# Kernel tuning notes

Hardware: AMD Instinct MI355X
Metric: run time of the kernel (lower is better)

## Reference

```python
import jax, jax.numpy as jnp
from jax import lax
import numpy as np

NUM_CAPS = 4
CAP_DIM = 8
NUM_CLASSES = 10
CLASS_DIM = 16


def squash(x):
    # x: [..., D]; scale = |x|^2/(1+|x|^2)/sqrt(|x|^2+1e-8)
    sq = jnp.sum(x * x, axis=-1, keepdims=True)
    return sq / (1.0 + sq) / jnp.sqrt(sq + 1e-8) * x


def primary_caps(x, w, b):
    # x: [B,C,H,W], w: [32,C,3,3] -> caps [B, H*W*NUM_CAPS, CAP_DIM]
    out = lax.conv_general_dilated(
        x, w, window_strides=(1, 1), padding=[(1, 1), (1, 1)],
        dimension_numbers=('NCHW', 'OIHW', 'NCHW')) + b[None, :, None, None]
    B, C, H, W = out.shape
    out = out.reshape(B, NUM_CAPS, CAP_DIM, H * W)
    out = out.transpose(0, 3, 1, 2).reshape(B, H * W * NUM_CAPS, CAP_DIM)
    return squash(out)


def setup_inputs() -> dict:
    key = jax.random.key(0)
    ks = jax.random.split(key, 7)
    B, H, Wd = 64, 32, 32
    hsi_c, sar_c = 144, 4
    N = 2 * H * Wd * NUM_CAPS  # 8192
    return {
        'x_hsi': jax.random.normal(ks[0], (B, hsi_c, H, Wd), jnp.float32),
        'x_sar': jax.random.normal(ks[1], (B, sar_c, H, Wd), jnp.float32),
        'wh': jax.random.normal(ks[2], (NUM_CAPS * CAP_DIM, hsi_c, 3, 3), jnp.float32) * 0.05,
        'bh': jax.random.normal(ks[3], (NUM_CAPS * CAP_DIM,), jnp.float32) * 0.05,
        'ws': jax.random.normal(ks[4], (NUM_CAPS * CAP_DIM, sar_c, 3, 3), jnp.float32) * 0.05,
        'bs': jax.random.normal(ks[5], (NUM_CAPS * CAP_DIM,), jnp.float32) * 0.05,
        'W': jax.random.normal(ks[6], (N, NUM_CLASSES, CLASS_DIM, CAP_DIM), jnp.float32),
    }


def reference(x_hsi, x_sar, wh, bh, ws, bs, W):
    caps_h = primary_caps(x_hsi, wh, bh)
    caps_s = primary_caps(x_sar, ws, bs)
    caps = jnp.concatenate([caps_h, caps_s], axis=1)  # [B, N, D]
    N = caps.shape[1]
    # routing_iters=1 with b=0 => c = 1/N uniform; s = sum_n c*u_hat = mean_n u_hat
    # u_hat[b,n,c,j] = sum_d W[n,c,j,d] * caps[b,n,d] (fused, never materialized)
    s = jnp.einsum('bnd,ncjd->bcj', caps, W) / N  # [B, num_classes, class_dim]
    v = squash(s)
    logits = jnp.sqrt(jnp.sum(v * v, axis=-1))  # [B, num_classes]
    return logits
```

## Files before the change

kernel.cpp:

```cpp
#include <hip/hip_runtime.h>
#include <hip/hip_bf16.h>


typedef __attribute__((ext_vector_type(8))) short bf16x8s;
typedef __attribute__((ext_vector_type(4))) float f32x4;

__device__ inline short f2bf(float f) {
    __hip_bfloat16 h = __float2bfloat16(f);
    return *reinterpret_cast<short*>(&h);
}

#define XPLANE 1156
#define XB_B (20 * XPLANE * 8)

__global__ __launch_bounds__(256) void prep_kernel(
        const float* __restrict__ wh, short* __restrict__ wtb2,
        const float* __restrict__ x_hsi, short* __restrict__ xb2,
        const float* __restrict__ wsar, float* __restrict__ wt_s) {
    int t = threadIdx.x;
    if (blockIdx.x < 180) {
        int idx = blockIdx.x * 256 + t;
        int tap = idx / 5120;
        int r2 = idx - tap * 5120;
        int cb = r2 >> 8;
        int oc = (r2 >> 3) & 31;
        int d = r2 & 7;
        int ch = cb * 8 + d;
        short v = 0;
        if (ch < 144) v = f2bf(wh[(oc * 144 + ch) * 9 + tap]);
        wtb2[idx] = v;
        return;
    }
    if (blockIdx.x == 2356) {
        for (int idx = t; idx < 1152; idx += 256) {
            int oc = idx & 31;
            int rest = idx >> 5;
            int tap = rest % 9;
            int cin = rest / 9;
            wt_s[cin * 288 + tap * 32 + oc] = wsar[(oc * 4 + cin) * 9 + tap];
        }
        return;
    }
    int blk = blockIdx.x - 180;
    int b = blk / 34;
    int y_o = blk - b * 34;
    bool yok = (y_o >= 1) && (y_o <= 32);
    int iy = y_o - 1;
    short* dstb = xb2 + (size_t)b * XB_B;
    for (int item = t; item < 680; item += 256) {
        int cb = item / 34;
        int xx = item - cb * 34;
        bf16x8s v = {0, 0, 0, 0, 0, 0, 0, 0};
        if (yok && xx >= 1 && xx <= 32 && cb < 18) {
            int x = xx - 1;
            #pragma unroll
            for (int d = 0; d < 8; ++d) {
                int ch = cb * 8 + d;
                v[d] = f2bf(x_hsi[(((size_t)b * 144 + ch) * 32 + iy) * 32 + x]);
            }
        }
        *(bf16x8s*)(dstb + ((size_t)(cb * 34 + y_o) * 34 + xx) * 8) = v;
    }
}

__global__ __launch_bounds__(256) void conv_both_kernel(
        const float* __restrict__ x_sar, const short* __restrict__ xb2,
        const short* __restrict__ wtb2, const float* __restrict__ bh,
        const float* __restrict__ wt_s, const float* __restrict__ bs,
        short* __restrict__ capsb) {
    __shared__ float ct[64][34];
    int t = threadIdx.x;

    if (blockIdx.x < 1024) {
        int l = t & 63;
        int wv = t >> 6;
        int mhalf = wv >> 1;
        int nt = wv & 1;
        int l15 = l & 15, lhi = l >> 4;
        int b = blockIdx.x >> 4;
        int y0 = (blockIdx.x & 15) << 1;
        int y = y0 + mhalf;

        const short* xaBase = xb2 + (size_t)b * XB_B + (size_t)lhi * XPLANE * 8;
        const short* waBase = wtb2 + (size_t)lhi * 256 + (size_t)(nt * 16 + l15) * 8;

        f32x4 acc0 = {0.f, 0.f, 0.f, 0.f};
        f32x4 acc1 = {0.f, 0.f, 0.f, 0.f};

        #pragma unroll
        for (int tap = 0; tap < 9; ++tap) {
            int dy = tap / 3, dx = tap % 3;
            int pixoff = ((y + dy) * 34 + l15 + dx) * 8;
            #pragma unroll
            for (int kc = 0; kc < 5; ++kc) {
                const short* xa = xaBase + (size_t)kc * (4 * XPLANE * 8) + pixoff;
                bf16x8s a0 = *(const bf16x8s*)xa;
                bf16x8s a1 = *(const bf16x8s*)(xa + 16 * 8);
                bf16x8s bf = *(const bf16x8s*)(waBase + (size_t)(tap * 20 + kc * 4) * 256);
                acc0 = __builtin_amdgcn_mfma_f32_16x16x32_bf16(a0, bf, acc0, 0, 0, 0);
                acc1 = __builtin_amdgcn_mfma_f32_16x16x32_bf16(a1, bf, acc1, 0, 0, 0);
            }
        }

        #pragma unroll
        for (int r = 0; r < 4; ++r) {
            ct[mhalf * 32 + lhi * 4 + r][nt * 16 + l15] = acc0[r];
            ct[mhalf * 32 + 16 + lhi * 4 + r][nt * 16 + l15] = acc1[r];
        }
        __syncthreads();

        int p = t >> 2;
        int cap = t & 3;
        float s[8];
        float sq = 0.0f;
        #pragma unroll
        for (int d = 0; d < 8; ++d) {
            s[d] = ct[p][cap * 8 + d] + bh[cap * 8 + d];
            sq += s[d] * s[d];
        }
        float scale = sq / ((1.0f + sq) * sqrtf(sq + 1e-8f));
        int pix = (y0 + (p >> 5)) * 32 + (p & 31);
        int n = pix * 4 + cap;
        bf16x8s o;
        #pragma unroll
        for (int d = 0; d < 8; ++d) o[d] = f2bf(s[d] * scale);
        *(bf16x8s*)(capsb + ((size_t)b * 8192 + n) * 8) = o;
    } else {
        int px_global = (blockIdx.x - 1024) * 256 + t;
        int b = px_global >> 10;
        int p = px_global & 1023;
        int y = p >> 5, x = p & 31;

        float acc[32];
        #pragma unroll
        for (int oc = 0; oc < 32; ++oc) acc[oc] = bs[oc];

        for (int cin = 0; cin < 4; ++cin) {
            const float* xc = x_sar + ((size_t)b * 4 + cin) * 1024;
            const float* wc = wt_s + cin * 288;
            #pragma unroll
            for (int ky = 0; ky < 3; ++ky) {
                int iy = y + ky - 1;
                bool rowok = (iy >= 0) && (iy < 32);
                const float* xrow = xc + iy * 32;
                float v0 = (rowok && x > 0)  ? xrow[x - 1] : 0.0f;
                float v1 = rowok             ? xrow[x]     : 0.0f;
                float v2 = (rowok && x < 31) ? xrow[x + 1] : 0.0f;
                const float* wk = wc + ky * 96;
                #pragma unroll
                for (int oc = 0; oc < 32; ++oc)
                    acc[oc] += v0 * wk[oc] + v1 * wk[32 + oc] + v2 * wk[64 + oc];
            }
        }

        #pragma unroll
        for (int cap = 0; cap < 4; ++cap) {
            float sq = 0.0f;
            #pragma unroll
            for (int d = 0; d < 8; ++d) sq += acc[cap * 8 + d] * acc[cap * 8 + d];
            float scale = sq / ((1.0f + sq) * sqrtf(sq + 1e-8f));
            int n = 4096 + p * 4 + cap;
            bf16x8s o;
            #pragma unroll
            for (int d = 0; d < 8; ++d) o[d] = f2bf(acc[cap * 8 + d] * scale);
            *(bf16x8s*)(capsb + ((size_t)b * 8192 + n) * 8) = o;
        }
    }
}

__global__ __launch_bounds__(256) void routing_mfma_kernel(
        const short* __restrict__ capsb, const float* __restrict__ W,
        float* __restrict__ partials) {
    __shared__ union {
        short ct[32][64][8];
        float red[4][64][32];
    } sm;
    int t = threadIdx.x;
    int kc = blockIdx.x;
    int ntp = blockIdx.y;
    int n0 = kc * 32;

    {
        int b = t >> 2;
        int ng = t & 3;
        const short* src = capsb + ((size_t)b * 8192 + n0 + ng * 8) * 8;
        #pragma unroll
        for (int i = 0; i < 8; ++i) {
            bf16x8s v = *(const bf16x8s*)(src + i * 8);
            *(bf16x8s*)&sm.ct[ng * 8 + i][b][0] = v;
        }
    }
    __syncthreads();

    int l = t & 63;
    int wv = t >> 6;
    int l15 = l & 15, lhi = l >> 4;

    f32x4 acc[2][4];
    #pragma unroll
    for (int a = 0; a < 2; ++a)
        #pragma unroll
        for (int m = 0; m < 4; ++m) acc[a][m] = (f32x4){0.f, 0.f, 0.f, 0.f};

    #pragma unroll
    for (int ks = 0; ks < 2; ++ks) {
        int nl = (wv * 2 + ks) * 4 + lhi;
        int n = n0 + nl;
        const float* wp = W + ((size_t)n * 160 + ntp * 32 + l15) * 8;
        union { short s[8]; bf16x8s v; } bu[2];
        #pragma unroll
        for (int ntl = 0; ntl < 2; ++ntl) {
            const float* wq = wp + (size_t)ntl * 128;
            float4 w0 = *(const float4*)wq;
            float4 w1 = *(const float4*)(wq + 4);
            bu[ntl].s[0] = f2bf(w0.x); bu[ntl].s[1] = f2bf(w0.y);
            bu[ntl].s[2] = f2bf(w0.z); bu[ntl].s[3] = f2bf(w0.w);
            bu[ntl].s[4] = f2bf(w1.x); bu[ntl].s[5] = f2bf(w1.y);
            bu[ntl].s[6] = f2bf(w1.z); bu[ntl].s[7] = f2bf(w1.w);
        }
        bf16x8s af[4];
        #pragma unroll
        for (int mt = 0; mt < 4; ++mt)
            af[mt] = *(const bf16x8s*)&sm.ct[nl][mt * 16 + l15][0];
        #pragma unroll
        for (int ntl = 0; ntl < 2; ++ntl)
            #pragma unroll
            for (int mt = 0; mt < 4; ++mt)
                acc[ntl][mt] = __builtin_amdgcn_mfma_f32_16x16x32_bf16(
                    af[mt], bu[ntl].v, acc[ntl][mt], 0, 0, 0);
    }
    __syncthreads();

    #pragma unroll
    for (int ntl = 0; ntl < 2; ++ntl)
        #pragma unroll
        for (int mt = 0; mt < 4; ++mt)
            #pragma unroll
            for (int r = 0; r < 4; ++r)
                sm.red[wv][mt * 16 + lhi * 4 + r][ntl * 16 + l15] = acc[ntl][mt][r];
    __syncthreads();

    for (int idx = t; idx < 2048; idx += 256) {
        int b = idx >> 5, cjl = idx & 31;
        float sum = sm.red[0][b][cjl] + sm.red[1][b][cjl]
                  + sm.red[2][b][cjl] + sm.red[3][b][cjl];
        partials[(((size_t)kc * 5 + ntp) * 64 + b) * 32 + cjl] = sum;
    }
}

__global__ __launch_bounds__(256) void finalize_kernel(
        const float* __restrict__ partials, float* __restrict__ out) {
    __shared__ float s_sh[160];
    int t = threadIdx.x;
    int b = blockIdx.x;
    if (t < 160) {
        int ntp = t >> 5, cjl = t & 31;
        float s = 0.0f;
        #pragma unroll 8
        for (int kc = 0; kc < 256; ++kc)
            s += partials[(((size_t)kc * 5 + ntp) * 64 + b) * 32 + cjl];
        s_sh[ntp * 32 + cjl] = s * (1.0f / 8192.0f);
    }
    __syncthreads();
    if (t < 10) {
        float sq = 0.0f;
        #pragma unroll
        for (int j = 0; j < 16; ++j) {
            float v = s_sh[t * 16 + j];
            sq += v * v;
        }
        float scale = sq / ((1.0f + sq) * sqrtf(sq + 1e-8f));
        out[b * 10 + t] = sqrtf(sq) * scale;
    }
}

extern "C" void kernel_launch(void* const* d_in, const int* in_sizes, int n_in,
                              void* d_out, int out_size, void* d_ws, size_t ws_size,
                              hipStream_t stream) {
    const float* x_hsi = (const float*)d_in[0];
    const float* x_sar = (const float*)d_in[1];
    const float* wh    = (const float*)d_in[2];
    const float* bh    = (const float*)d_in[3];
    const float* wsar  = (const float*)d_in[4];
    const float* bs    = (const float*)d_in[5];
    const float* W     = (const float*)d_in[6];
    float* out = (float*)d_out;

    char* ws = (char*)d_ws;
    short* wtb2     = (short*)(ws + 0);
    float* wt_s     = (float*)(ws + 98304);
    short* xb2      = (short*)(ws + 131072);
    float* partials = (float*)(ws + 131072);
    short* capsb    = (short*)(ws + 23805952);

    prep_kernel<<<2357, 256, 0, stream>>>(wh, wtb2, x_hsi, xb2, wsar, wt_s);

    conv_both_kernel<<<1280, 256, 0, stream>>>(x_sar, xb2, wtb2, bh, wt_s, bs, capsb);

    routing_mfma_kernel<<<dim3(256, 5), 256, 0, stream>>>(capsb, W, partials);

    finalize_kernel<<<64, 256, 0, stream>>>(partials, out);
}
```

Before: 77.78 us.

## Stage conv input halo in LDS and retile HSI conv to 4 rows per block

```diff
diff --git a/kernel.cpp b/kernel.cpp
--- a/kernel.cpp
+++ b/kernel.cpp
@@ -17,6 +17,7 @@
         const float* __restrict__ wh, short* __restrict__ wtb2,
         const float* __restrict__ x_hsi, short* __restrict__ xb2,
         const float* __restrict__ wsar, float* __restrict__ wt_s) {
+    __shared__ short tile[144][33];
     int t = threadIdx.x;
     if (blockIdx.x < 180) {
         int idx = blockIdx.x * 256 + t;
@@ -46,6 +47,13 @@
     int y_o = blk - b * 34;
     bool yok = (y_o >= 1) && (y_o <= 32);
     int iy = y_o - 1;
+    if (yok) {
+        for (int base = 0; base < 144; base += 8) {
+            int ch = base + (t >> 5), x = t & 31;
+            tile[ch][x] = f2bf(x_hsi[(((size_t)b * 144 + ch) * 32 + iy) * 32 + x]);
+        }
+    }
+    __syncthreads();
     short* dstb = xb2 + (size_t)b * XB_B;
     for (int item = t; item < 680; item += 256) {
         int cb = item / 34;
@@ -54,10 +62,7 @@
         if (yok && xx >= 1 && xx <= 32 && cb < 18) {
             int x = xx - 1;
             #pragma unroll
-            for (int d = 0; d < 8; ++d) {
-                int ch = cb * 8 + d;
-                v[d] = f2bf(x_hsi[(((size_t)b * 144 + ch) * 32 + iy) * 32 + x]);
-            }
+            for (int d = 0; d < 8; ++d) v[d] = tile[cb * 8 + d][x];
         }
         *(bf16x8s*)(dstb + ((size_t)(cb * 34 + y_o) * 34 + xx) * 8) = v;
     }
@@ -68,65 +73,83 @@
         const short* __restrict__ wtb2, const float* __restrict__ bh,
         const float* __restrict__ wt_s, const float* __restrict__ bs,
         short* __restrict__ capsb) {
-    __shared__ float ct[64][34];
+    __shared__ union {
+        short xs[20][6][34][8];
+        float ct[128][33];
+    } sm;
     int t = threadIdx.x;
 
-    if (blockIdx.x < 1024) {
+    if (blockIdx.x < 512) {
+        int b = blockIdx.x >> 3;
+        int y0 = (blockIdx.x & 7) << 2;
+
+        const short* src = xb2 + (size_t)b * XB_B;
+        for (int i = t; i < 4080; i += 256) {
+            int cb = i / 204;
+            int rem = i - cb * 204;
+            int row = rem / 34;
+            int xx = rem - row * 34;
+            bf16x8s v = *(const bf16x8s*)(src + ((size_t)(cb * 34 + y0 + row) * 34 + xx) * 8);
+            *(bf16x8s*)&sm.xs[cb][row][xx][0] = v;
+        }
+        __syncthreads();
+
         int l = t & 63;
         int wv = t >> 6;
-        int mhalf = wv >> 1;
-        int nt = wv & 1;
         int l15 = l & 15, lhi = l >> 4;
-        int b = blockIdx.x >> 4;
-        int y0 = (blockIdx.x & 15) << 1;
-        int y = y0 + mhalf;
-
-        const short* xaBase = xb2 + (size_t)b * XB_B + (size_t)lhi * XPLANE * 8;
-        const short* waBase = wtb2 + (size_t)lhi * 256 + (size_t)(nt * 16 + l15) * 8;
-
-        f32x4 acc0 = {0.f, 0.f, 0.f, 0.f};
-        f32x4 acc1 = {0.f, 0.f, 0.f, 0.f};
+
+        f32x4 acc[2][2] = {{{0.f,0.f,0.f,0.f},{0.f,0.f,0.f,0.f}},
+                           {{0.f,0.f,0.f,0.f},{0.f,0.f,0.f,0.f}}};
 
         #pragma unroll
         for (int tap = 0; tap < 9; ++tap) {
             int dy = tap / 3, dx = tap % 3;
-            int pixoff = ((y + dy) * 34 + l15 + dx) * 8;
             #pragma unroll
             for (int kc = 0; kc < 5; ++kc) {
-                const short* xa = xaBase + (size_t)kc * (4 * XPLANE * 8) + pixoff;
-                bf16x8s a0 = *(const bf16x8s*)xa;
-                bf16x8s a1 = *(const bf16x8s*)(xa + 16 * 8);
-                bf16x8s bf = *(const bf16x8s*)(waBase + (size_t)(tap * 20 + kc * 4) * 256);
-                acc0 = __builtin_amdgcn_mfma_f32_16x16x32_bf16(a0, bf, acc0, 0, 0, 0);
-                acc1 = __builtin_amdgcn_mfma_f32_16x16x32_bf16(a1, bf, acc1, 0, 0, 0);
+                bf16x8s a0 = *(const bf16x8s*)&sm.xs[kc * 4 + lhi][wv + dy][l15 + dx][0];
+                bf16x8s a1 = *(const bf16x8s*)&sm.xs[kc * 4 + lhi][wv + dy][16 + l15 + dx][0];
+                const short* wa = wtb2 + ((size_t)(tap * 20 + kc * 4 + lhi) * 32 + l15) * 8;
+                bf16x8s b0 = *(const bf16x8s*)wa;
+                bf16x8s b1 = *(const bf16x8s*)(wa + 128);
+                acc[0][0] = __builtin_amdgcn_mfma_f32_16x16x32_bf16(a0, b0, acc[0][0], 0, 0, 0);
+                acc[0][1] = __builtin_amdgcn_mfma_f32_16x16x32_bf16(a0, b1, acc[0][1], 0, 0, 0);
+                acc[1][0] = __builtin_amdgcn_mfma_f32_16x16x32_bf16(a1, b0, acc[1][0], 0, 0, 0);
+                acc[1][1] = __builtin_amdgcn_mfma_f32_16x16x32_bf16(a1, b1, acc[1][1], 0, 0, 0);
             }
         }
-
-        #pragma unroll
-        for (int r = 0; r < 4; ++r) {
-            ct[mhalf * 32 + lhi * 4 + r][nt * 16 + l15] = acc0[r];
-            ct[mhalf * 32 + 16 + lhi * 4 + r][nt * 16 + l15] = acc1[r];
-        }
         __syncthreads();
 
-        int p = t >> 2;
-        int cap = t & 3;
-        float s[8];
-        float sq = 0.0f;
-        #pragma unroll
-        for (int d = 0; d < 8; ++d) {
-            s[d] = ct[p][cap * 8 + d] + bh[cap * 8 + d];
-            sq += s[d] * s[d];
-        }
-        float scale = sq / ((1.0f + sq) * sqrtf(sq + 1e-8f));
-        int pix = (y0 + (p >> 5)) * 32 + (p & 31);
-        int n = pix * 4 + cap;
-        bf16x8s o;
-        #pragma unroll
-        for (int d = 0; d < 8; ++d) o[d] = f2bf(s[d] * scale);
-        *(bf16x8s*)(capsb + ((size_t)b * 8192 + n) * 8) = o;
+        #pragma unroll
+        for (int xh = 0; xh < 2; ++xh)
+            #pragma unroll
+            for (int nt = 0; nt < 2; ++nt)
+                #pragma unroll
+                for (int r = 0; r < 4; ++r)
+                    sm.ct[wv * 32 + xh * 16 + lhi * 4 + r][nt * 16 + l15] = acc[xh][nt][r];
+        __syncthreads();
+
+        #pragma unroll
+        for (int h = 0; h < 2; ++h) {
+            int q = t + h * 256;
+            int p = q >> 2;
+            int cap = q & 3;
+            float s[8];
+            float sq = 0.0f;
+            #pragma unroll
+            for (int d = 0; d < 8; ++d) {
+                s[d] = sm.ct[p][cap * 8 + d] + bh[cap * 8 + d];
+                sq += s[d] * s[d];
+            }
+            float scale = sq / ((1.0f + sq) * sqrtf(sq + 1e-8f));
+            int pix = (y0 + (p >> 5)) * 32 + (p & 31);
+            int n = pix * 4 + cap;
+            bf16x8s o;
+            #pragma unroll
+            for (int d = 0; d < 8; ++d) o[d] = f2bf(s[d] * scale);
+            *(bf16x8s*)(capsb + ((size_t)b * 8192 + n) * 8) = o;
+        }
     } else {
-        int px_global = (blockIdx.x - 1024) * 256 + t;
+        int px_global = (blockIdx.x - 512) * 256 + t;
         int b = px_global >> 10;
         int p = px_global & 1023;
         int y = p >> 5, x = p & 31;
@@ -295,7 +318,7 @@
 
     prep_kernel<<<2357, 256, 0, stream>>>(wh, wtb2, x_hsi, xb2, wsar, wt_s);
 
-    conv_both_kernel<<<1280, 256, 0, stream>>>(x_sar, xb2, wtb2, bh, wt_s, bs, capsb);
+    conv_both_kernel<<<768, 256, 0, stream>>>(x_sar, xb2, wtb2, bh, wt_s, bs, capsb);
 
     routing_mfma_kernel<<<dim3(256, 5), 256, 0, stream>>>(capsb, W, partials);
 
```

New measurement: 78.85 us. No clear change (+1.4%).

## Stage HSI input rows in LDS for conv and move SAR conv into prep kernel

Applied to the files above, without the earlier changes.

```diff
diff --git a/kernel.cpp b/kernel.cpp
--- a/kernel.cpp
+++ b/kernel.cpp
@@ -10,14 +10,20 @@
     return *reinterpret_cast<short*>(&h);
 }
 
-#define XPLANE 1156
-#define XB_B (20 * XPLANE * 8)
+#define XB_B (20 * 1156 * 8)
+#define PLANE_SH 1090
 
 __global__ __launch_bounds__(256) void prep_kernel(
         const float* __restrict__ wh, short* __restrict__ wtb2,
         const float* __restrict__ x_hsi, short* __restrict__ xb2,
-        const float* __restrict__ wsar, float* __restrict__ wt_s) {
+        const float* __restrict__ x_sar, const float* __restrict__ wsar,
+        const float* __restrict__ bs, short* __restrict__ capsb) {
+    __shared__ union {
+        short tile[144][33];
+        float wt_lds[1152];
+    } sm;
     int t = threadIdx.x;
+
     if (blockIdx.x < 180) {
         int idx = blockIdx.x * 256 + t;
         int tap = idx / 5120;
@@ -31,102 +37,18 @@
         wtb2[idx] = v;
         return;
     }
-    if (blockIdx.x == 2356) {
-        for (int idx = t; idx < 1152; idx += 256) {
-            int oc = idx & 31;
-            int rest = idx >> 5;
-            int tap = rest % 9;
-            int cin = rest / 9;
-            wt_s[cin * 288 + tap * 32 + oc] = wsar[(oc * 4 + cin) * 9 + tap];
-        }
-        return;
-    }
-    int blk = blockIdx.x - 180;
-    int b = blk / 34;
-    int y_o = blk - b * 34;
-    bool yok = (y_o >= 1) && (y_o <= 32);
-    int iy = y_o - 1;
-    short* dstb = xb2 + (size_t)b * XB_B;
-    for (int item = t; item < 680; item += 256) {
-        int cb = item / 34;
-        int xx = item - cb * 34;
-        bf16x8s v = {0, 0, 0, 0, 0, 0, 0, 0};
-        if (yok && xx >= 1 && xx <= 32 && cb < 18) {
-            int x = xx - 1;
-            #pragma unroll
-            for (int d = 0; d < 8; ++d) {
-                int ch = cb * 8 + d;
-                v[d] = f2bf(x_hsi[(((size_t)b * 144 + ch) * 32 + iy) * 32 + x]);
-            }
-        }
-        *(bf16x8s*)(dstb + ((size_t)(cb * 34 + y_o) * 34 + xx) * 8) = v;
-    }
-}
-
-__global__ __launch_bounds__(256) void conv_both_kernel(
-        const float* __restrict__ x_sar, const short* __restrict__ xb2,
-        const short* __restrict__ wtb2, const float* __restrict__ bh,
-        const float* __restrict__ wt_s, const float* __restrict__ bs,
-        short* __restrict__ capsb) {
-    __shared__ float ct[64][34];
-    int t = threadIdx.x;
-
-    if (blockIdx.x < 1024) {
-        int l = t & 63;
-        int wv = t >> 6;
-        int mhalf = wv >> 1;
-        int nt = wv & 1;
-        int l15 = l & 15, lhi = l >> 4;
-        int b = blockIdx.x >> 4;
-        int y0 = (blockIdx.x & 15) << 1;
-        int y = y0 + mhalf;
-
-        const short* xaBase = xb2 + (size_t)b * XB_B + (size_t)lhi * XPLANE * 8;
-        const short* waBase = wtb2 + (size_t)lhi * 256 + (size_t)(nt * 16 + l15) * 8;
-
-        f32x4 acc0 = {0.f, 0.f, 0.f, 0.f};
-        f32x4 acc1 = {0.f, 0.f, 0.f, 0.f};
-
-        #pragma unroll
-        for (int tap = 0; tap < 9; ++tap) {
-            int dy = tap / 3, dx = tap % 3;
-            int pixoff = ((y + dy) * 34 + l15 + dx) * 8;
-            #pragma unroll
-            for (int kc = 0; kc < 5; ++kc) {
-                const short* xa = xaBase + (size_t)kc * (4 * XPLANE * 8) + pixoff;
-                bf16x8s a0 = *(const bf16x8s*)xa;
-                bf16x8s a1 = *(const bf16x8s*)(xa + 16 * 8);
-                bf16x8s bf = *(const bf16x8s*)(waBase + (size_t)(tap * 20 + kc * 4) * 256);
-                acc0 = __builtin_amdgcn_mfma_f32_16x16x32_bf16(a0, bf, acc0, 0, 0, 0);
-                acc1 = __builtin_amdgcn_mfma_f32_16x16x32_bf16(a1, bf, acc1, 0, 0, 0);
-            }
-        }
-
-        #pragma unroll
-        for (int r = 0; r < 4; ++r) {
-            ct[mhalf * 32 + lhi * 4 + r][nt * 16 + l15] = acc0[r];
-            ct[mhalf * 32 + 16 + lhi * 4 + r][nt * 16 + l15] = acc1[r];
+
+    if (blockIdx.x >= 2356) {
+        for (int i = t; i < 1152; i += 256) {
+            int oc = i / 36;
+            int r = i - oc * 36;
+            int cin = r / 9;
+            int tap = r - cin * 9;
+            sm.wt_lds[cin * 288 + tap * 32 + oc] = wsar[i];
         }
         __syncthreads();
 
-        int p = t >> 2;
-        int cap = t & 3;
-        float s[8];
-        float sq = 0.0f;
-        #pragma unroll
-        for (int d = 0; d < 8; ++d) {
-            s[d] = ct[p][cap * 8 + d] + bh[cap * 8 + d];
-            sq += s[d] * s[d];
-        }
-        float scale = sq / ((1.0f + sq) * sqrtf(sq + 1e-8f));
-        int pix = (y0 + (p >> 5)) * 32 + (p & 31);
-        int n = pix * 4 + cap;
-        bf16x8s o;
-        #pragma unroll
-        for (int d = 0; d < 8; ++d) o[d] = f2bf(s[d] * scale);
-        *(bf16x8s*)(capsb + ((size_t)b * 8192 + n) * 8) = o;
-    } else {
-        int px_global = (blockIdx.x - 1024) * 256 + t;
+        int px_global = (blockIdx.x - 2356) * 256 + t;
         int b = px_global >> 10;
         int p = px_global & 1023;
         int y = p >> 5, x = p & 31;
@@ -137,7 +59,7 @@
 
         for (int cin = 0; cin < 4; ++cin) {
             const float* xc = x_sar + ((size_t)b * 4 + cin) * 1024;
-            const float* wc = wt_s + cin * 288;
+            const float* wc = &sm.wt_lds[cin * 288];
             #pragma unroll
             for (int ky = 0; ky < 3; ++ky) {
                 int iy = y + ky - 1;
@@ -165,7 +87,104 @@
             for (int d = 0; d < 8; ++d) o[d] = f2bf(acc[cap * 8 + d] * scale);
             *(bf16x8s*)(capsb + ((size_t)b * 8192 + n) * 8) = o;
         }
-    }
+        return;
+    }
+
+    int blk = blockIdx.x - 180;
+    int b = blk / 34;
+    int y_o = blk - b * 34;
+    bool yok = (y_o >= 1) && (y_o <= 32);
+    int iy = y_o - 1;
+    if (yok) {
+        for (int base = 0; base < 144; base += 8) {
+            int ch = base + (t >> 5), x = t & 31;
+            sm.tile[ch][x] = f2bf(x_hsi[(((size_t)b * 144 + ch) * 32 + iy) * 32 + x]);
+        }
+    }
+    __syncthreads();
+    short* dstb = xb2 + (size_t)b * XB_B;
+    for (int item = t; item < 680; item += 256) {
+        int cb = item / 34;
+        int xx = item - cb * 34;
+        bf16x8s v = {0, 0, 0, 0, 0, 0, 0, 0};
+        if (yok && xx >= 1 && xx <= 32 && cb < 18) {
+            int x = xx - 1;
+            #pragma unroll
+            for (int d = 0; d < 8; ++d) v[d] = sm.tile[cb * 8 + d][x];
+        }
+        *(bf16x8s*)(dstb + ((size_t)(cb * 34 + y_o) * 34 + xx) * 8) = v;
+    }
+}
+
+__global__ __launch_bounds__(256) void conv_hsi_kernel(
+        const short* __restrict__ xb2, const short* __restrict__ wtb2,
+        const float* __restrict__ bh, short* __restrict__ capsb) {
+    __shared__ union {
+        short xs[20 * PLANE_SH];
+        float ct[64][33];
+    } sm;
+    int t = threadIdx.x;
+    int b = blockIdx.x >> 4;
+    int y0 = (blockIdx.x & 15) << 1;
+
+    const short* src = xb2 + (size_t)b * XB_B + y0 * 272;
+    for (int i = t; i < 2720; i += 256) {
+        int cb = i / 136;
+        int rem = i - cb * 136;
+        bf16x8s v = *(const bf16x8s*)(src + (size_t)cb * 9248 + rem * 8);
+        *(bf16x8s*)&sm.xs[cb * PLANE_SH + rem * 8] = v;
+    }
+    __syncthreads();
+
+    int l = t & 63;
+    int wv = t >> 6;
+    int wr = wv >> 1;
+    int xh = wv & 1;
+    int l15 = l & 15, lhi = l >> 4;
+
+    f32x4 acc0 = {0.f, 0.f, 0.f, 0.f};
+    f32x4 acc1 = {0.f, 0.f, 0.f, 0.f};
+
+    #pragma unroll
+    for (int tap = 0; tap < 9; ++tap) {
+        int dy = tap / 3, dx = tap % 3;
+        int arow = ((wr + dy) * 34 + xh * 16 + l15 + dx) * 8;
+        #pragma unroll
+        for (int kc = 0; kc < 5; ++kc) {
+            bf16x8s a = *(const bf16x8s*)&sm.xs[(kc * 4 + lhi) * PLANE_SH + arow];
+            const short* wa = wtb2 + ((size_t)(tap * 20 + kc * 4 + lhi) * 32 + l15) * 8;
+            bf16x8s b0 = *(const bf16x8s*)wa;
+            bf16x8s b1 = *(const bf16x8s*)(wa + 128);
+            acc0 = __builtin_amdgcn_mfma_f32_16x16x32_bf16(a, b0, acc0, 0, 0, 0);
+            acc1 = __builtin_amdgcn_mfma_f32_16x16x32_bf16(a, b1, acc1, 0, 0, 0);
+        }
+    }
+    __syncthreads();
+
+    #pragma unroll
+    for (int r = 0; r < 4; ++r) {
+        int px = wr * 32 + xh * 16 + lhi * 4 + r;
+        sm.ct[px][l15] = acc0[r];
+        sm.ct[px][16 + l15] = acc1[r];
+    }
+    __syncthreads();
+
+    int p = t >> 2;
+    int cap = t & 3;
+    float s[8];
+    float sq = 0.0f;
+    #pragma unroll
+    for (int d = 0; d < 8; ++d) {
+        s[d] = sm.ct[p][cap * 8 + d] + bh[cap * 8 + d];
+        sq += s[d] * s[d];
+    }
+    float scale = sq / ((1.0f + sq) * sqrtf(sq + 1e-8f));
+    int pix = (y0 + (p >> 5)) * 32 + (p & 31);
+    int n = pix * 4 + cap;
+    bf16x8s o;
+    #pragma unroll
+    for (int d = 0; d < 8; ++d) o[d] = f2bf(s[d] * scale);
+    *(bf16x8s*)(capsb + ((size_t)b * 8192 + n) * 8) = o;
 }
 
 __global__ __launch_bounds__(256) void routing_mfma_kernel(
@@ -288,14 +307,13 @@
 
     char* ws = (char*)d_ws;
     short* wtb2     = (short*)(ws + 0);
-    float* wt_s     = (float*)(ws + 98304);
     short* xb2      = (short*)(ws + 131072);
     float* partials = (float*)(ws + 131072);
     short* capsb    = (short*)(ws + 23805952);
 
-    prep_kernel<<<2357, 256, 0, stream>>>(wh, wtb2, x_hsi, xb2, wsar, wt_s);
-
-    conv_both_kernel<<<1280, 256, 0, stream>>>(x_sar, xb2, wtb2, bh, wt_s, bs, capsb);
+    prep_kernel<<<2612, 256, 0, stream>>>(wh, wtb2, x_hsi, xb2, x_sar, wsar, bs, capsb);
+
+    conv_hsi_kernel<<<1024, 256, 0, stream>>>(xb2, wtb2, bh, capsb);
 
     routing_mfma_kernel<<<dim3(256, 5), 256, 0, stream>>>(capsb, W, partials);
 
```

Measured after the change: 76.81 us. About the same (-1.2%).
